# Kernel optimization log

Measured on AMD Instinct MI355X. Metric: run time of the kernel, lower is better.

The kernel has to match this reference:

```python
import jax, jax.numpy as jnp
import numpy as np

D_MODEL, N_HEADS, LATENT, ROPE = 4096, 128, 512, 64
HEAD_DIM = D_MODEL // N_HEADS  # 32
B, S = 2, 1024


def setup_inputs() -> dict:
    key = jax.random.key(0)
    ks = jax.random.split(key, 9)
    def w(k, i, o):
        return jax.random.normal(k, (i, o), dtype=jnp.float32) * (1.0 / np.sqrt(i))
    return {
        "x": jax.random.normal(ks[0], (B, S, D_MODEL), dtype=jnp.float32),
        "Wq_down": w(ks[1], D_MODEL, LATENT),
        "Wq_up": w(ks[2], LATENT, N_HEADS * HEAD_DIM),
        "Wq_rope": w(ks[3], D_MODEL, N_HEADS * ROPE),
        "Wkv_down": w(ks[4], D_MODEL, LATENT),
        "Wk_up": w(ks[5], LATENT, N_HEADS * HEAD_DIM),
        "Wv_up": w(ks[6], LATENT, N_HEADS * HEAD_DIM),
        "Wk_rope": w(ks[7], D_MODEL, ROPE),
        "Wo": w(ks[8], N_HEADS * HEAD_DIM, D_MODEL),
    }


def reference(x, Wq_down, Wq_up, Wq_rope, Wkv_down, Wk_up, Wv_up, Wk_rope, Wo):
    b, s, _ = x.shape
    # latent down-projections
    c_q = x @ Wq_down                                   # [B,S,latent]
    c_kv = x @ Wkv_down                                 # [B,S,latent]
    # up-projections, reshaped to per-head
    q_c = (c_q @ Wq_up).reshape(b, s, N_HEADS, HEAD_DIM)    # [B,S,H,Dh]
    q_r = (x @ Wq_rope).reshape(b, s, N_HEADS, ROPE)        # [B,S,H,Dr]
    k_c = (c_kv @ Wk_up).reshape(b, s, N_HEADS, HEAD_DIM)   # [B,S,H,Dh]
    v_c = (c_kv @ Wv_up).reshape(b, s, N_HEADS, HEAD_DIM)   # [B,S,H,Dh]
    k_r = x @ Wk_rope                                       # [B,S,Dr] shared over heads
    scale = jnp.asarray((HEAD_DIM + ROPE) ** 0.5, x.dtype)
    # scores = q.k with q=[q_c|q_r], k=[k_c|k_r(broadcast)] -> split the dot product
    scores = (jnp.einsum("bqhd,bkhd->bhqk", q_c, k_c)
              + jnp.einsum("bqhd,bkd->bhqk", q_r, k_r)) / scale  # [B,H,S,S]
    attn = jax.nn.softmax(scores, axis=-1)
    out = jnp.einsum("bhqk,bkhd->bqhd", attn, v_c)          # [B,S,H,Dh]
    out = out.reshape(b, s, N_HEADS * HEAD_DIM)
    return out @ Wo                                         # [B,S,d_model]
```

## Files before the change

kernel.cpp:

```cpp
#include <hip/hip_runtime.h>
#include <hip/hip_bf16.h>
#include <math.h>

#define D_MODEL 4096
#define N_HEADS 128
#define LATENT  512
#define ROPE_D  64
#define HEAD_D  32
#define BATCH   2
#define SEQ     1024
#define NTOK    (BATCH*SEQ)

typedef unsigned short u16;
typedef __attribute__((ext_vector_type(8))) short bf16x8;
typedef __attribute__((ext_vector_type(4))) float f32x4;

__device__ __forceinline__ u16 f2bf(float f) {
    union { float f; unsigned u; } v; v.f = f;
    unsigned r = (v.u + 0x7fffu + ((v.u >> 16) & 1u)) >> 16;
    return (u16)r;
}

__device__ __forceinline__ void gl_lds16(const u16* g, u16* l) {
    __builtin_amdgcn_global_load_lds(
        (const __attribute__((address_space(1))) unsigned int*)g,
        (__attribute__((address_space(3))) unsigned int*)l, 16, 0, 0);
}

__device__ __forceinline__ void castT_tile(const float* __restrict__ W,
                                           u16* __restrict__ Wt,
                                           int K, int N, int jx, int jy,
                                           float (*tile)[33])
{
    const int tid = threadIdx.x;
    const int j0 = jx * 32, i0 = jy * 32;
    {
        int r = tid >> 3, c4 = (tid & 7) << 2;
        float4 v = *(const float4*)(W + (size_t)(i0 + r) * N + j0 + c4);
        tile[r][c4 + 0] = v.x; tile[r][c4 + 1] = v.y;
        tile[r][c4 + 2] = v.z; tile[r][c4 + 3] = v.w;
    }
    __syncthreads();
    {
        int n = tid >> 3, k4 = (tid & 7) << 2;
        u16 o[4] = { f2bf(tile[k4 + 0][n]), f2bf(tile[k4 + 1][n]),
                     f2bf(tile[k4 + 2][n]), f2bf(tile[k4 + 3][n]) };
        *(uint2*)(Wt + (size_t)(j0 + n) * K + i0 + k4) = *(uint2*)o;
    }
}

__device__ __forceinline__ void gemm_core(const u16* __restrict__ A,
                                          const u16* __restrict__ Bt,
                                          void* __restrict__ Cout,
                                          int N, int K, int lda, int ldb, int ldc,
                                          int bm, int bn, u16* As, u16* Bs,
                                          int OUTF32)
{
    const int tid  = threadIdx.x;
    const int lane = tid & 63;
    const int wave = tid >> 6;
    const int wr = wave >> 1, wc = wave & 1;
    const int l15 = lane & 15, lg = lane >> 4;

    f32x4 acc[4][4];
    #pragma unroll
    for (int i = 0; i < 4; ++i)
        #pragma unroll
        for (int j = 0; j < 4; ++j) acc[i][j] = (f32x4){0.f, 0.f, 0.f, 0.f};

    for (int kt = 0; kt < K; kt += 64) {
        __syncthreads();
        #pragma unroll
        for (int i = 0; i < 4; ++i) {
            int f = i * 256 + tid;
            int row = f >> 3, c = f & 7;
            int sc = c ^ (row & 7);
            gl_lds16(A + (size_t)(bm + row) * lda + kt + sc * 8, As + f * 8);
        }
        #pragma unroll
        for (int i = 0; i < 4; ++i) {
            int f = i * 256 + tid;
            int row = f >> 3, c = f & 7;
            int sc = c ^ (row & 7);
            gl_lds16(Bt + (size_t)(bn + row) * ldb + kt + sc * 8, Bs + f * 8);
        }
        __syncthreads();

        #pragma unroll
        for (int t = 0; t < 2; ++t) {
            bf16x8 af[4], bf[4];
            #pragma unroll
            for (int fm = 0; fm < 4; ++fm) {
                int row = wr * 64 + fm * 16 + l15;
                int c = (t * 4 + lg) ^ (row & 7);
                af[fm] = *(const bf16x8*)(As + row * 64 + c * 8);
            }
            #pragma unroll
            for (int fn = 0; fn < 4; ++fn) {
                int row = wc * 64 + fn * 16 + l15;
                int c = (t * 4 + lg) ^ (row & 7);
                bf[fn] = *(const bf16x8*)(Bs + row * 64 + c * 8);
            }
            #pragma unroll
            for (int fm = 0; fm < 4; ++fm)
                #pragma unroll
                for (int fn = 0; fn < 4; ++fn)
                    acc[fm][fn] = __builtin_amdgcn_mfma_f32_16x16x32_bf16(
                        af[fm], bf[fn], acc[fm][fn], 0, 0, 0);
        }
    }

    #pragma unroll
    for (int fm = 0; fm < 4; ++fm)
        #pragma unroll
        for (int fn = 0; fn < 4; ++fn)
            #pragma unroll
            for (int ri = 0; ri < 4; ++ri) {
                int row = bm + wr * 64 + fm * 16 + 4 * lg + ri;
                int col = bn + wc * 64 + fn * 16 + l15;
                float v = acc[fm][fn][ri];
                if (OUTF32) ((float*)Cout)[(size_t)row * ldc + col] = v;
                else        ((u16*)Cout)[(size_t)row * ldc + col] = f2bf(v);
            }
}

template<int OUTF32>
__global__ __launch_bounds__(256)
void gemm_bf16(const u16* __restrict__ A, const u16* __restrict__ Bt,
               void* __restrict__ Cout, int N, int K,
               int lda, int ldb, int ldc)
{
    __shared__ __align__(16) u16 As[128 * 64];
    __shared__ __align__(16) u16 Bs[128 * 64];
    const int nwg  = gridDim.x * gridDim.y;
    const int orig = blockIdx.y * gridDim.x + blockIdx.x;
    const int swz  = (orig & 7) * (nwg >> 3) + (orig >> 3);
    const int bm = (swz % gridDim.y) * 128;
    const int bn = (swz / gridDim.y) * 128;
    gemm_core(A, Bt, Cout, N, K, lda, ldb, ldc, bm, bn, As, Bs, OUTF32);
}

__global__ __launch_bounds__(256)
void prep_kernel(const float* __restrict__ x, u16* __restrict__ xb,
                 const float* __restrict__ Wq_rope, const float* __restrict__ Wq_down,
                 const float* __restrict__ Wkv_down, const float* __restrict__ Wk_rope,
                 const float* __restrict__ Wk_up, const float* __restrict__ Wv_up,
                 const float* __restrict__ Wq_up,
                 u16* __restrict__ BigT, u16* __restrict__ UpT, u16* __restrict__ WuqT)
{
    __shared__ float tile[32][33];
    const int tid = threadIdx.x;
    int id = blockIdx.x;
    if (id < 4096) {
        size_t i = ((size_t)id * 256 + tid) * 8;
        float4 a = *(const float4*)(x + i);
        float4 b = *(const float4*)(x + i + 4);
        u16 o[8] = {f2bf(a.x), f2bf(a.y), f2bf(a.z), f2bf(a.w),
                    f2bf(b.x), f2bf(b.y), f2bf(b.z), f2bf(b.w)};
        *(bf16x8*)(xb + i) = *(bf16x8*)o;
        return;
    }
    id -= 4096;
    if (id < 32768) { castT_tile(Wq_rope, BigT, 4096, 8192, id & 255, id >> 8, tile); return; }
    id -= 32768;
    if (id < 2048) { castT_tile(Wq_down, BigT + (size_t)8192 * 4096, 4096, 512, id & 15, id >> 4, tile); return; }
    id -= 2048;
    if (id < 2048) { castT_tile(Wkv_down, BigT + (size_t)8704 * 4096, 4096, 512, id & 15, id >> 4, tile); return; }
    id -= 2048;
    if (id < 256) { castT_tile(Wk_rope, BigT + (size_t)9216 * 4096, 4096, 64, id & 1, id >> 1, tile); return; }
    id -= 256;
    if (id < 2048) { castT_tile(Wk_up, UpT, 512, 4096, id & 127, id >> 7, tile); return; }
    id -= 2048;
    if (id < 2048) { castT_tile(Wv_up, UpT + (size_t)4096 * 512, 512, 4096, id & 127, id >> 7, tile); return; }
    id -= 2048;
    if (id < 2048) { castT_tile(Wq_up, WuqT, 512, 4096, id & 127, id >> 7, tile); return; }
    id -= 2048;
    {
        u16* dst = BigT + ((size_t)9280 + id) * 4096;
        bf16x8 z = (bf16x8){0, 0, 0, 0, 0, 0, 0, 0};
        *(bf16x8*)(dst + tid * 8) = z;
        *(bf16x8*)(dst + 2048 + tid * 8) = z;
    }
}

__global__ __launch_bounds__(256)
void fused2_kernel(const u16* __restrict__ Cbig, const u16* __restrict__ UpT,
                   u16* __restrict__ C2, const u16* __restrict__ WuqT,
                   u16* __restrict__ q_c, const float* __restrict__ Wo,
                   u16* __restrict__ WoT)
{
    __shared__ __align__(16) u16 As[128 * 64];
    __shared__ __align__(16) u16 Bs[128 * 64];
    int id = blockIdx.x;
    if (id < 1024) {
        const int swz = (id & 7) * 128 + (id >> 3);
        const int bm = (swz & 15) * 128, bn = (swz >> 4) * 128;
        gemm_core(Cbig + 8704, UpT, C2, 8192, 512, 9344, 512, 8192, bm, bn, As, Bs, 0);
        return;
    }
    id -= 1024;
    if (id < 512) {
        const int swz = (id & 7) * 64 + (id >> 3);
        const int bm = (swz & 15) * 128, bn = (swz >> 4) * 128;
        gemm_core(Cbig + 8192, WuqT, q_c, 4096, 512, 9344, 512, 4096, bm, bn, As, Bs, 0);
        return;
    }
    id -= 512;
    {
        float (*tile)[33] = reinterpret_cast<float(*)[33]>(As);
        castT_tile(Wo, WoT, 4096, 4096, id & 127, id >> 7, tile);
    }
}

__global__ __launch_bounds__(256)
void vtrans_kernel(const u16* __restrict__ vc, u16* __restrict__ vt)
{
    __shared__ __align__(16) u16 tile[64][72];
    const int tid = threadIdx.x;
    const int c0 = blockIdx.x * 64;
    const int s0 = blockIdx.y * 64;
    const int b  = blockIdx.z;
    #pragma unroll
    for (int it = 0; it < 2; ++it) {
        int e = it * 256 + tid;
        int r = e >> 3, c8 = e & 7;
        *(bf16x8*)&tile[r][c8 * 8] =
            *(const bf16x8*)(vc + (size_t)(b * SEQ + s0 + r) * 8192 + c0 + c8 * 8);
    }
    __syncthreads();
    #pragma unroll
    for (int it = 0; it < 2; ++it) {
        int e = it * 256 + tid;
        int d = e >> 3, c8 = e & 7;
        u16 o[8];
        #pragma unroll
        for (int j = 0; j < 8; ++j) o[j] = tile[c8 * 8 + j][d];
        *(bf16x8*)(vt + (size_t)(b * D_MODEL + c0 + d) * SEQ + s0 + c8 * 8) = *(bf16x8*)o;
    }
}

__global__ __launch_bounds__(256)
void attn_kernel(const u16* __restrict__ q_c, const u16* __restrict__ q_r,
                 const u16* __restrict__ k_c, const u16* __restrict__ k_r,
                 const u16* __restrict__ vt,  u16* __restrict__ attn_out)
{
    __shared__ __align__(16) u16 s_kc[2][64 * 32];
    __shared__ __align__(16) u16 s_kr[2][64 * 64];
    __shared__ __align__(16) u16 s_vt[2][32 * 64];
    __shared__ __align__(16) u16 s_p[4][16 * 64];

    const int tid  = threadIdx.x;
    const int lane = tid & 63;
    const int w    = tid >> 6;
    const int l15  = lane & 15, lg = lane >> 4;
    const int q0 = blockIdx.x * 64;
    const int h  = blockIdx.y;
    const int b  = blockIdx.z;
    const size_t bS = (size_t)b * SEQ;
    const int hc = h * HEAD_D;
    const float c2 = 0.1020620726159658f * 1.44269504088896f;

    const int qrow = q0 + w * 16 + l15;
    const bf16x8 qf0 = *(const bf16x8*)(q_c + (bS + qrow) * 4096 + hc + lg * 8);
    const bf16x8 qf1 = *(const bf16x8*)(q_r + (bS + qrow) * 9344 + h * ROPE_D + lg * 8);
    const bf16x8 qf2 = *(const bf16x8*)(q_r + (bS + qrow) * 9344 + h * ROPE_D + 32 + lg * 8);

    float m2 = -1e30f, lsum = 0.f;
    f32x4 oacc[2];
    oacc[0] = (f32x4){0.f, 0.f, 0.f, 0.f};
    oacc[1] = (f32x4){0.f, 0.f, 0.f, 0.f};

    auto stage = [&](int buf, int k0) {
        { int f = tid, r = f >> 2, c = f & 3;
          gl_lds16(k_c + (bS + k0 + r) * 8192 + hc + ((c ^ (r & 3)) << 3),
                   &s_kc[buf][f * 8]); }
        #pragma unroll
        for (int it = 0; it < 2; ++it) {
          int f = it * 256 + tid, r = f >> 3, c = f & 7;
          gl_lds16(k_r + (bS + k0 + r) * 9344 + ((c ^ (r & 7)) << 3),
                   &s_kr[buf][f * 8]); }
        { int f = tid, d = f >> 3, c = f & 7;
          gl_lds16(vt + ((size_t)b * D_MODEL + hc + d) * SEQ + k0 + ((c ^ (d & 7)) << 3),
                   &s_vt[buf][f * 8]); }
    };

    stage(0, 0);
    asm volatile("s_waitcnt vmcnt(0)" ::: "memory");
    __builtin_amdgcn_sched_barrier(0);
    __builtin_amdgcn_s_barrier();
    __builtin_amdgcn_sched_barrier(0);

    int cur = 0;
    for (int t = 0; t < SEQ / 64; ++t) {
        if (t + 1 < SEQ / 64) {
            stage(cur ^ 1, (t + 1) * 64);
            asm volatile("s_waitcnt vmcnt(4)" ::: "memory");
        } else {
            asm volatile("s_waitcnt vmcnt(0)" ::: "memory");
        }
        __builtin_amdgcn_sched_barrier(0);
        __builtin_amdgcn_s_barrier();
        __builtin_amdgcn_sched_barrier(0);

        f32x4 sc[4];
        #pragma unroll
        for (int fc = 0; fc < 4; ++fc) sc[fc] = (f32x4){0.f, 0.f, 0.f, 0.f};
        __builtin_amdgcn_s_setprio(1);
        #pragma unroll
        for (int fc = 0; fc < 4; ++fc) {
            int row = fc * 16 + l15;
            bf16x8 kb = *(const bf16x8*)&s_kc[cur][row * 32 + ((lg ^ (row & 3)) << 3)];
            sc[fc] = __builtin_amdgcn_mfma_f32_16x16x32_bf16(kb, qf0, sc[fc], 0, 0, 0);
        }
        #pragma unroll
        for (int tt = 0; tt < 2; ++tt) {
            bf16x8 qf = tt ? qf2 : qf1;
            #pragma unroll
            for (int fc = 0; fc < 4; ++fc) {
                int row = fc * 16 + l15;
                bf16x8 kb = *(const bf16x8*)&s_kr[cur][row * 64 + (((tt * 4 + lg) ^ (row & 7)) << 3)];
                sc[fc] = __builtin_amdgcn_mfma_f32_16x16x32_bf16(kb, qf, sc[fc], 0, 0, 0);
            }
        }
        __builtin_amdgcn_s_setprio(0);

        float tmx = sc[0][0];
        #pragma unroll
        for (int fc = 0; fc < 4; ++fc)
            #pragma unroll
            for (int ri = 0; ri < 4; ++ri)
                tmx = fmaxf(tmx, sc[fc][ri]);
        tmx = fmaxf(tmx, __shfl_xor(tmx, 16));
        tmx = fmaxf(tmx, __shfl_xor(tmx, 32));
        float tl2 = tmx * c2;
        if (!__all(tl2 <= m2 + 8.f)) {
            float mn = fmaxf(m2, tl2);
            float corr = exp2f(m2 - mn);
            m2 = mn;
            lsum *= corr;
            #pragma unroll
            for (int ri = 0; ri < 4; ++ri) {
                float cr = __shfl(corr, 4 * lg + ri);
                oacc[0][ri] *= cr; oacc[1][ri] *= cr;
            }
        }
        float rs = 0.f;
        unsigned pk0[4], pk1[4];
        #pragma unroll
        for (int fc = 0; fc < 4; ++fc) {
            float p0 = exp2f(fmaf(sc[fc][0], c2, -m2));
            float p1 = exp2f(fmaf(sc[fc][1], c2, -m2));
            float p2 = exp2f(fmaf(sc[fc][2], c2, -m2));
            float p3 = exp2f(fmaf(sc[fc][3], c2, -m2));
            rs += (p0 + p1) + (p2 + p3);
            asm("v_cvt_pk_bf16_f32 %0, %1, %2" : "=v"(pk0[fc]) : "v"(p0), "v"(p1));
            asm("v_cvt_pk_bf16_f32 %0, %1, %2" : "=v"(pk1[fc]) : "v"(p2), "v"(p3));
        }
        rs += __shfl_xor(rs, 16);
        rs += __shfl_xor(rs, 32);
        lsum += rs;
        #pragma unroll
        for (int fc = 0; fc < 4; ++fc) {
            int ch = (2 * fc + (lg >> 1)) ^ (l15 & 7);
            *(uint2*)&s_p[w][l15 * 64 + ch * 8 + 4 * (lg & 1)] =
                make_uint2(pk0[fc], pk1[fc]);
        }

        __builtin_amdgcn_s_setprio(1);
        #pragma unroll
        for (int t2 = 0; t2 < 2; ++t2) {
            bf16x8 pa = *(const bf16x8*)&s_p[w][l15 * 64 + (((t2 * 4 + lg) ^ (l15 & 7)) << 3)];
            #pragma unroll
            for (int fd = 0; fd < 2; ++fd) {
                int row = fd * 16 + l15;
                bf16x8 vb = *(const bf16x8*)&s_vt[cur][row * 64 + (((t2 * 4 + lg) ^ (row & 7)) << 3)];
                oacc[fd] = __builtin_amdgcn_mfma_f32_16x16x32_bf16(pa, vb, oacc[fd], 0, 0, 0);
            }
        }
        __builtin_amdgcn_s_setprio(0);

        asm volatile("s_waitcnt lgkmcnt(0)" ::: "memory");
        __builtin_amdgcn_sched_barrier(0);
        __builtin_amdgcn_s_barrier();
        __builtin_amdgcn_sched_barrier(0);
        cur ^= 1;
    }

    #pragma unroll
    for (int ri = 0; ri < 4; ++ri) {
        float ls = __shfl(lsum, 4 * lg + ri);
        float inv = 1.f / ls;
        int row = q0 + w * 16 + 4 * lg + ri;
        attn_out[(bS + row) * 4096 + hc + l15]      = f2bf(oacc[0][ri] * inv);
        attn_out[(bS + row) * 4096 + hc + 16 + l15] = f2bf(oacc[1][ri] * inv);
    }
}

extern "C" void kernel_launch(void* const* d_in, const int* in_sizes, int n_in,
                              void* d_out, int out_size, void* d_ws, size_t ws_size,
                              hipStream_t stream)
{
    (void)in_sizes; (void)n_in; (void)out_size; (void)ws_size;

    const float* x        = (const float*)d_in[0];
    const float* Wq_down  = (const float*)d_in[1];
    const float* Wq_up    = (const float*)d_in[2];
    const float* Wq_rope  = (const float*)d_in[3];
    const float* Wkv_down = (const float*)d_in[4];
    const float* Wk_up    = (const float*)d_in[5];
    const float* Wv_up    = (const float*)d_in[6];
    const float* Wk_rope  = (const float*)d_in[7];
    const float* Wo       = (const float*)d_in[8];

    u16* ws   = (u16*)d_ws;
    u16* xb   = ws;
    u16* BigT = xb + (size_t)8388608;
    u16* UpT  = BigT + (size_t)38797312;
    u16* WuqT = UpT + (size_t)4194304;
    u16* C_big= WuqT + (size_t)2097152;
    u16* C2   = C_big + (size_t)19136512;
    u16* WoT  = BigT;
    u16* vt   = BigT + (size_t)16777216;
    u16* q_c  = BigT + (size_t)25165824;
    u16* attn_out = xb;

    dim3 blk(256);

    hipLaunchKernelGGL(prep_kernel, dim3(47424), blk, 0, stream,
                       x, xb, Wq_rope, Wq_down, Wkv_down, Wk_rope,
                       Wk_up, Wv_up, Wq_up, BigT, UpT, WuqT);
    gemm_bf16<0><<<dim3(73, 16), blk, 0, stream>>>(
        xb, BigT, C_big, 9344, 4096, 4096, 4096, 9344);
    hipLaunchKernelGGL(fused2_kernel, dim3(1024 + 512 + 16384), blk, 0, stream,
                       C_big, UpT, C2, WuqT, q_c, Wo, WoT);
    hipLaunchKernelGGL(vtrans_kernel, dim3(64, 16, 2), blk, 0, stream, C2 + 4096, vt);
    hipLaunchKernelGGL(attn_kernel, dim3(16, 128, 2), blk, 0, stream,
                       q_c, C_big, C2, C_big + 9216, vt, attn_out);
    gemm_bf16<1><<<dim3(32, 16), blk, 0, stream>>>(
        attn_out, WoT, d_out, 4096, 4096, 4096, 4096, 4096);
}
```

Baseline: 512.7 us.

## Fuse V transpose into up-projection GEMM epilogue and drop vtrans kernel

The K/V up-projection GEMM now writes K directly into a compact 4096-wide buffer and writes V already transposed into the vt layout from its epilogue. This removes the separate vtrans kernel launch along with its extra read and write of V. The attention kernel's K row stride changes to match. The transposed V stores are 8-byte scattered writes along the sequence dimension, which may coalesce less well. The tile max reduction in attention is also rewritten as a shallower tree.

```diff
diff --git a/kernel.cpp b/kernel.cpp
--- a/kernel.cpp
+++ b/kernel.cpp
@@ -49,12 +49,13 @@
     }
 }
 
+template<int MODE>
 __device__ __forceinline__ void gemm_core(const u16* __restrict__ A,
                                           const u16* __restrict__ Bt,
                                           void* __restrict__ Cout,
                                           int N, int K, int lda, int ldb, int ldc,
                                           int bm, int bn, u16* As, u16* Bs,
-                                          int OUTF32)
+                                          u16* __restrict__ vtp)
 {
     const int tid  = threadIdx.x;
     const int lane = tid & 63;
@@ -113,18 +114,38 @@
     #pragma unroll
     for (int fm = 0; fm < 4; ++fm)
         #pragma unroll
-        for (int fn = 0; fn < 4; ++fn)
-            #pragma unroll
-            for (int ri = 0; ri < 4; ++ri) {
-                int row = bm + wr * 64 + fm * 16 + 4 * lg + ri;
-                int col = bn + wc * 64 + fn * 16 + l15;
-                float v = acc[fm][fn][ri];
-                if (OUTF32) ((float*)Cout)[(size_t)row * ldc + col] = v;
-                else        ((u16*)Cout)[(size_t)row * ldc + col] = f2bf(v);
-            }
-}
-
-template<int OUTF32>
+        for (int fn = 0; fn < 4; ++fn) {
+            int row0 = bm + wr * 64 + fm * 16 + 4 * lg;
+            int col  = bn + wc * 64 + fn * 16 + l15;
+            if (MODE == 2) {
+                if (col < 4096) {
+                    #pragma unroll
+                    for (int ri = 0; ri < 4; ++ri)
+                        ((u16*)Cout)[(size_t)(row0 + ri) * 4096 + col] =
+                            f2bf(acc[fm][fn][ri]);
+                } else {
+                    int d = col - 4096;
+                    int b = row0 >> 10, s = row0 & 1023;
+                    u16 o[4] = {f2bf(acc[fm][fn][0]), f2bf(acc[fm][fn][1]),
+                                f2bf(acc[fm][fn][2]), f2bf(acc[fm][fn][3])};
+                    *(uint2*)(vtp + ((size_t)b * 4096 + d) * 1024 + s) = *(uint2*)o;
+                }
+            } else {
+                if (col < N) {
+                    #pragma unroll
+                    for (int ri = 0; ri < 4; ++ri) {
+                        float v = acc[fm][fn][ri];
+                        if (MODE == 1)
+                            ((float*)Cout)[(size_t)(row0 + ri) * ldc + col] = v;
+                        else
+                            ((u16*)Cout)[(size_t)(row0 + ri) * ldc + col] = f2bf(v);
+                    }
+                }
+            }
+        }
+}
+
+template<int MODE>
 __global__ __launch_bounds__(256)
 void gemm_bf16(const u16* __restrict__ A, const u16* __restrict__ Bt,
                void* __restrict__ Cout, int N, int K,
@@ -137,7 +158,7 @@
     const int swz  = (orig & 7) * (nwg >> 3) + (orig >> 3);
     const int bm = (swz % gridDim.y) * 128;
     const int bn = (swz / gridDim.y) * 128;
-    gemm_core(A, Bt, Cout, N, K, lda, ldb, ldc, bm, bn, As, Bs, OUTF32);
+    gemm_core<MODE>(A, Bt, Cout, N, K, lda, ldb, ldc, bm, bn, As, Bs, nullptr);
 }
 
 __global__ __launch_bounds__(256)
@@ -185,9 +206,9 @@
 
 __global__ __launch_bounds__(256)
 void fused2_kernel(const u16* __restrict__ Cbig, const u16* __restrict__ UpT,
-                   u16* __restrict__ C2, const u16* __restrict__ WuqT,
-                   u16* __restrict__ q_c, const float* __restrict__ Wo,
-                   u16* __restrict__ WoT)
+                   u16* __restrict__ k_c, u16* __restrict__ vt,
+                   const u16* __restrict__ WuqT, u16* __restrict__ q_c,
+                   const float* __restrict__ Wo, u16* __restrict__ WoT)
 {
     __shared__ __align__(16) u16 As[128 * 64];
     __shared__ __align__(16) u16 Bs[128 * 64];
@@ -195,47 +216,20 @@
     if (id < 1024) {
         const int swz = (id & 7) * 128 + (id >> 3);
         const int bm = (swz & 15) * 128, bn = (swz >> 4) * 128;
-        gemm_core(Cbig + 8704, UpT, C2, 8192, 512, 9344, 512, 8192, bm, bn, As, Bs, 0);
+        gemm_core<2>(Cbig + 8704, UpT, k_c, 8192, 512, 9344, 512, 4096, bm, bn, As, Bs, vt);
         return;
     }
     id -= 1024;
     if (id < 512) {
         const int swz = (id & 7) * 64 + (id >> 3);
         const int bm = (swz & 15) * 128, bn = (swz >> 4) * 128;
-        gemm_core(Cbig + 8192, WuqT, q_c, 4096, 512, 9344, 512, 4096, bm, bn, As, Bs, 0);
+        gemm_core<0>(Cbig + 8192, WuqT, q_c, 4096, 512, 9344, 512, 4096, bm, bn, As, Bs, nullptr);
         return;
     }
     id -= 512;
     {
         float (*tile)[33] = reinterpret_cast<float(*)[33]>(As);
         castT_tile(Wo, WoT, 4096, 4096, id & 127, id >> 7, tile);
-    }
-}
-
-__global__ __launch_bounds__(256)
-void vtrans_kernel(const u16* __restrict__ vc, u16* __restrict__ vt)
-{
-    __shared__ __align__(16) u16 tile[64][72];
-    const int tid = threadIdx.x;
-    const int c0 = blockIdx.x * 64;
-    const int s0 = blockIdx.y * 64;
-    const int b  = blockIdx.z;
-    #pragma unroll
-    for (int it = 0; it < 2; ++it) {
-        int e = it * 256 + tid;
-        int r = e >> 3, c8 = e & 7;
-        *(bf16x8*)&tile[r][c8 * 8] =
-            *(const bf16x8*)(vc + (size_t)(b * SEQ + s0 + r) * 8192 + c0 + c8 * 8);
-    }
-    __syncthreads();
-    #pragma unroll
-    for (int it = 0; it < 2; ++it) {
-        int e = it * 256 + tid;
-        int d = e >> 3, c8 = e & 7;
-        u16 o[8];
-        #pragma unroll
-        for (int j = 0; j < 8; ++j) o[j] = tile[c8 * 8 + j][d];
-        *(bf16x8*)(vt + (size_t)(b * D_MODEL + c0 + d) * SEQ + s0 + c8 * 8) = *(bf16x8*)o;
     }
 }
 
@@ -272,7 +266,7 @@
 
     auto stage = [&](int buf, int k0) {
         { int f = tid, r = f >> 2, c = f & 3;
-          gl_lds16(k_c + (bS + k0 + r) * 8192 + hc + ((c ^ (r & 3)) << 3),
+          gl_lds16(k_c + (bS + k0 + r) * 4096 + hc + ((c ^ (r & 3)) << 3),
                    &s_kc[buf][f * 8]); }
         #pragma unroll
         for (int it = 0; it < 2; ++it) {
@@ -324,12 +318,14 @@
         }
         __builtin_amdgcn_s_setprio(0);
 
-        float tmx = sc[0][0];
-        #pragma unroll
-        for (int fc = 0; fc < 4; ++fc)
-            #pragma unroll
-            for (int ri = 0; ri < 4; ++ri)
-                tmx = fmaxf(tmx, sc[fc][ri]);
+        float a0 = fmaxf(fmaxf(sc[0][0], sc[0][1]), sc[0][2]);
+        float a1 = fmaxf(fmaxf(sc[0][3], sc[1][0]), sc[1][1]);
+        float a2 = fmaxf(fmaxf(sc[1][2], sc[1][3]), sc[2][0]);
+        float a3 = fmaxf(fmaxf(sc[2][1], sc[2][2]), sc[2][3]);
+        float a4 = fmaxf(fmaxf(sc[3][0], sc[3][1]), sc[3][2]);
+        float b0 = fmaxf(fmaxf(a0, a1), a2);
+        float b1 = fmaxf(fmaxf(a3, a4), sc[3][3]);
+        float tmx = fmaxf(b0, b1);
         tmx = fmaxf(tmx, __shfl_xor(tmx, 16));
         tmx = fmaxf(tmx, __shfl_xor(tmx, 32));
         float tl2 = tmx * c2;
@@ -418,7 +414,7 @@
     u16* UpT  = BigT + (size_t)38797312;
     u16* WuqT = UpT + (size_t)4194304;
     u16* C_big= WuqT + (size_t)2097152;
-    u16* C2   = C_big + (size_t)19136512;
+    u16* kc   = C_big + (size_t)19136512;
     u16* WoT  = BigT;
     u16* vt   = BigT + (size_t)16777216;
     u16* q_c  = BigT + (size_t)25165824;
@@ -432,10 +428,9 @@
     gemm_bf16<0><<<dim3(73, 16), blk, 0, stream>>>(
         xb, BigT, C_big, 9344, 4096, 4096, 4096, 9344);
     hipLaunchKernelGGL(fused2_kernel, dim3(1024 + 512 + 16384), blk, 0, stream,
-                       C_big, UpT, C2, WuqT, q_c, Wo, WoT);
-    hipLaunchKernelGGL(vtrans_kernel, dim3(64, 16, 2), blk, 0, stream, C2 + 4096, vt);
+                       C_big, UpT, kc, vt, WuqT, q_c, Wo, WoT);
     hipLaunchKernelGGL(attn_kernel, dim3(16, 128, 2), blk, 0, stream,
-                       q_c, C_big, C2, C_big + 9216, vt, attn_out);
+                       q_c, C_big, kc, C_big + 9216, vt, attn_out);
     gemm_bf16<1><<<dim3(32, 16), blk, 0, stream>>>(
         attn_out, WoT, d_out, 4096, 4096, 4096, 4096, 4096);
 }
```

Result: slower. 527.2 us (+2.8%).

## Add 256x256 multi-buffered GEMM for the big fused projection and split off remainder

Applied to the files above, without the earlier changes.

Adds a new 512-thread GEMM kernel with 256x256 tiles and a four-slot LDS ring of K-halves, loaded asynchronously via global_load_lds with explicit vmcnt waits and barriers. It covers the first 8192 columns of the large x-projection, and the remaining 1152 columns go to the existing 128x128 kernel, which gains a column bound check. Larger tiles raise data reuse per LDS load and overlap loads with MFMA work, at the cost of 128KB of LDS per block, low occupancy, and only 256 blocks. The attention row-max reduction is also rewritten as a tree to shorten the dependency chain.

```diff
diff --git a/kernel.cpp b/kernel.cpp
--- a/kernel.cpp
+++ b/kernel.cpp
@@ -49,12 +49,12 @@
     }
 }
 
+template<int MODE>
 __device__ __forceinline__ void gemm_core(const u16* __restrict__ A,
                                           const u16* __restrict__ Bt,
                                           void* __restrict__ Cout,
                                           int N, int K, int lda, int ldb, int ldc,
-                                          int bm, int bn, u16* As, u16* Bs,
-                                          int OUTF32)
+                                          int bm, int bn, u16* As, u16* Bs)
 {
     const int tid  = threadIdx.x;
     const int lane = tid & 63;
@@ -118,13 +118,15 @@
             for (int ri = 0; ri < 4; ++ri) {
                 int row = bm + wr * 64 + fm * 16 + 4 * lg + ri;
                 int col = bn + wc * 64 + fn * 16 + l15;
-                float v = acc[fm][fn][ri];
-                if (OUTF32) ((float*)Cout)[(size_t)row * ldc + col] = v;
-                else        ((u16*)Cout)[(size_t)row * ldc + col] = f2bf(v);
-            }
-}
-
-template<int OUTF32>
+                if (col < N) {
+                    float v = acc[fm][fn][ri];
+                    if (MODE == 1) ((float*)Cout)[(size_t)row * ldc + col] = v;
+                    else           ((u16*)Cout)[(size_t)row * ldc + col] = f2bf(v);
+                }
+            }
+}
+
+template<int MODE>
 __global__ __launch_bounds__(256)
 void gemm_bf16(const u16* __restrict__ A, const u16* __restrict__ Bt,
                void* __restrict__ Cout, int N, int K,
@@ -137,7 +139,123 @@
     const int swz  = (orig & 7) * (nwg >> 3) + (orig >> 3);
     const int bm = (swz % gridDim.y) * 128;
     const int bn = (swz / gridDim.y) * 128;
-    gemm_core(A, Bt, Cout, N, K, lda, ldb, ldc, bm, bn, As, Bs, OUTF32);
+    gemm_core<MODE>(A, Bt, Cout, N, K, lda, ldb, ldc, bm, bn, As, Bs);
+}
+
+__global__ __launch_bounds__(512)
+void gemm256(const u16* __restrict__ A, const u16* __restrict__ Bt,
+             u16* __restrict__ Cout, int N, int K,
+             int lda, int ldb, int ldc)
+{
+    constexpr int SLOT = 16384;
+    extern __shared__ __align__(16) u16 lds[];
+
+    const int tid  = threadIdx.x;
+    const int lane = tid & 63, wave = tid >> 6;
+    const int wr = wave >> 2, wc = wave & 3;
+    const int l15 = lane & 15, lg = lane >> 4;
+
+    const int nwg  = gridDim.x * gridDim.y;
+    const int orig = blockIdx.y * gridDim.x + blockIdx.x;
+    const int swz  = (orig & 7) * (nwg >> 3) + (orig >> 3);
+    const int bm = (swz % gridDim.y) * 256;
+    const int bn = (swz / gridDim.y) * 256;
+
+    const int NH = K >> 5;
+    const int NT = NH >> 1;
+
+    auto stage_unit = [&](int u) {
+        const int h = u >> 1, op = u & 1;
+        u16* base = lds + (h & 3) * SLOT + op * 8192;
+        const u16* G = op ? Bt : A;
+        const int ldg  = op ? ldb : lda;
+        const int boff = op ? bn : bm;
+        const int kh = h << 5;
+        #pragma unroll
+        for (int it = 0; it < 2; ++it) {
+            int f = it * 512 + tid;
+            int row = f >> 2, c = f & 3;
+            int gc = c ^ ((row >> 1) & 3);
+            gl_lds16(G + (size_t)(boff + row) * ldg + kh + gc * 8, base + f * 8);
+        }
+    };
+
+    f32x4 acc[8][4];
+    #pragma unroll
+    for (int m = 0; m < 8; ++m)
+        #pragma unroll
+        for (int n = 0; n < 4; ++n) acc[m][n] = (f32x4){0.f, 0.f, 0.f, 0.f};
+
+    #pragma unroll
+    for (int u = 0; u < 6; ++u) stage_unit(u);
+    asm volatile("s_waitcnt vmcnt(4)" ::: "memory");
+    __builtin_amdgcn_sched_barrier(0);
+    __builtin_amdgcn_s_barrier();
+    __builtin_amdgcn_sched_barrier(0);
+
+    for (int t = 0; t < NT; ++t) {
+        #pragma unroll
+        for (int hh = 0; hh < 2; ++hh) {
+            const int h = 2 * t + hh;
+            const u16* As_ = lds + (h & 3) * SLOT;
+            const u16* Bs_ = As_ + 8192;
+            bf16x8 bfr[4];
+            #pragma unroll
+            for (int sub = 0; sub < 2; ++sub) {
+                bf16x8 af[4];
+                #pragma unroll
+                for (int mm = 0; mm < 4; ++mm) {
+                    int row = wr * 128 + (sub * 4 + mm) * 16 + l15;
+                    af[mm] = *(const bf16x8*)(As_ + row * 32 +
+                                              ((lg ^ ((row >> 1) & 3)) << 3));
+                }
+                if (sub == 0) {
+                    #pragma unroll
+                    for (int nn = 0; nn < 4; ++nn) {
+                        int row = wc * 64 + nn * 16 + l15;
+                        bfr[nn] = *(const bf16x8*)(Bs_ + row * 32 +
+                                                   ((lg ^ ((row >> 1) & 3)) << 3));
+                    }
+                }
+                {
+                    int u = 4 * t + 6 + 2 * hh + sub;
+                    if (u < 2 * NH) stage_unit(u);
+                }
+                if (hh == 1 && sub == 1 && t + 1 < NT) {
+                    int iss = 4 * t + 10; if (iss > 2 * NH) iss = 2 * NH;
+                    int ru = iss - (4 * t + 8);
+                    if (ru >= 2) asm volatile("s_waitcnt vmcnt(4)" ::: "memory");
+                    else         asm volatile("s_waitcnt vmcnt(0)" ::: "memory");
+                }
+                __builtin_amdgcn_sched_barrier(0);
+                __builtin_amdgcn_s_barrier();
+                __builtin_amdgcn_sched_barrier(0);
+                __builtin_amdgcn_s_setprio(1);
+                #pragma unroll
+                for (int mm = 0; mm < 4; ++mm)
+                    #pragma unroll
+                    for (int nn = 0; nn < 4; ++nn)
+                        acc[sub * 4 + mm][nn] = __builtin_amdgcn_mfma_f32_16x16x32_bf16(
+                            af[mm], bfr[nn], acc[sub * 4 + mm][nn], 0, 0, 0);
+                __builtin_amdgcn_s_setprio(0);
+                __builtin_amdgcn_sched_barrier(0);
+                __builtin_amdgcn_s_barrier();
+                __builtin_amdgcn_sched_barrier(0);
+            }
+        }
+    }
+
+    #pragma unroll
+    for (int m = 0; m < 8; ++m)
+        #pragma unroll
+        for (int n = 0; n < 4; ++n)
+            #pragma unroll
+            for (int ri = 0; ri < 4; ++ri) {
+                int row = bm + wr * 128 + m * 16 + 4 * lg + ri;
+                int col = bn + wc * 64 + n * 16 + l15;
+                if (col < N)
+                    Cout[(size_t)row * ldc + col] = f2bf(acc[m][n][ri]);
+            }
 }
 
 __global__ __launch_bounds__(256)
@@ -195,14 +313,14 @@
     if (id < 1024) {
         const int swz = (id & 7) * 128 + (id >> 3);
         const int bm = (swz & 15) * 128, bn = (swz >> 4) * 128;
-        gemm_core(Cbig + 8704, UpT, C2, 8192, 512, 9344, 512, 8192, bm, bn, As, Bs, 0);
+        gemm_core<0>(Cbig + 8704, UpT, C2, 8192, 512, 9344, 512, 8192, bm, bn, As, Bs);
         return;
     }
     id -= 1024;
     if (id < 512) {
         const int swz = (id & 7) * 64 + (id >> 3);
         const int bm = (swz & 15) * 128, bn = (swz >> 4) * 128;
-        gemm_core(Cbig + 8192, WuqT, q_c, 4096, 512, 9344, 512, 4096, bm, bn, As, Bs, 0);
+        gemm_core<0>(Cbig + 8192, WuqT, q_c, 4096, 512, 9344, 512, 4096, bm, bn, As, Bs);
         return;
     }
     id -= 512;
@@ -324,12 +442,14 @@
         }
         __builtin_amdgcn_s_setprio(0);
 
-        float tmx = sc[0][0];
-        #pragma unroll
-        for (int fc = 0; fc < 4; ++fc)
-            #pragma unroll
-            for (int ri = 0; ri < 4; ++ri)
-                tmx = fmaxf(tmx, sc[fc][ri]);
+        float a0 = fmaxf(fmaxf(sc[0][0], sc[0][1]), sc[0][2]);
+        float a1 = fmaxf(fmaxf(sc[0][3], sc[1][0]), sc[1][1]);
+        float a2 = fmaxf(fmaxf(sc[1][2], sc[1][3]), sc[2][0]);
+        float a3 = fmaxf(fmaxf(sc[2][1], sc[2][2]), sc[2][3]);
+        float a4 = fmaxf(fmaxf(sc[3][0], sc[3][1]), sc[3][2]);
+        float b0 = fmaxf(fmaxf(a0, a1), a2);
+        float b1 = fmaxf(fmaxf(a3, a4), sc[3][3]);
+        float tmx = fmaxf(b0, b1);
         tmx = fmaxf(tmx, __shfl_xor(tmx, 16));
         tmx = fmaxf(tmx, __shfl_xor(tmx, 32));
         float tl2 = tmx * c2;
@@ -426,11 +546,16 @@
 
     dim3 blk(256);
 
+    (void)hipFuncSetAttribute((const void*)&gemm256,
+                              hipFuncAttributeMaxDynamicSharedMemorySize, 131072);
+
     hipLaunchKernelGGL(prep_kernel, dim3(47424), blk, 0, stream,
                        x, xb, Wq_rope, Wq_down, Wkv_down, Wk_rope,
                        Wk_up, Wv_up, Wq_up, BigT, UpT, WuqT);
-    gemm_bf16<0><<<dim3(73, 16), blk, 0, stream>>>(
-        xb, BigT, C_big, 9344, 4096, 4096, 4096, 9344);
+    gemm256<<<dim3(32, 8), dim3(512), 131072, stream>>>(
+        xb, BigT, C_big, 8192, 4096, 4096, 4096, 9344);
+    gemm_bf16<0><<<dim3(9, 16), blk, 0, stream>>>(
+        xb, BigT + (size_t)8192 * 4096, C_big + 8192, 1152, 4096, 4096, 4096, 9344);
     hipLaunchKernelGGL(fused2_kernel, dim3(1024 + 512 + 16384), blk, 0, stream,
                        C_big, UpT, C2, WuqT, q_c, Wo, WoT);
     hipLaunchKernelGGL(vtrans_kernel, dim3(64, 16, 2), blk, 0, stream, C2 + 4096, vt);
```

New measurement: 540.4 us. 1.05x slower.

## Compute softmax row sums via MFMA against ones column; change K-LDS swizzle

Applied to the files above, without the earlier changes.

Drops the per-tile VALU row-sum and its cross-lane shuffles in the attention kernel. The softmax denominator is now accumulated by an extra MFMA of the probability tile against an LDS ones matrix, so it sums the bf16-rounded probabilities used in P·V. The s_kc swizzle now uses (row>>1)&3 to cut LDS bank conflicts, and the tile max becomes a shallower tree. The GEMM core also gains a column bound check and a template mode parameter. The cost is one more MFMA and one more LDS read per inner step, plus a small extra LDS buffer.

```diff
diff --git a/kernel.cpp b/kernel.cpp
--- a/kernel.cpp
+++ b/kernel.cpp
@@ -49,12 +49,12 @@
     }
 }
 
+template<int MODE>
 __device__ __forceinline__ void gemm_core(const u16* __restrict__ A,
                                           const u16* __restrict__ Bt,
                                           void* __restrict__ Cout,
                                           int N, int K, int lda, int ldb, int ldc,
-                                          int bm, int bn, u16* As, u16* Bs,
-                                          int OUTF32)
+                                          int bm, int bn, u16* As, u16* Bs)
 {
     const int tid  = threadIdx.x;
     const int lane = tid & 63;
@@ -118,13 +118,15 @@
             for (int ri = 0; ri < 4; ++ri) {
                 int row = bm + wr * 64 + fm * 16 + 4 * lg + ri;
                 int col = bn + wc * 64 + fn * 16 + l15;
-                float v = acc[fm][fn][ri];
-                if (OUTF32) ((float*)Cout)[(size_t)row * ldc + col] = v;
-                else        ((u16*)Cout)[(size_t)row * ldc + col] = f2bf(v);
-            }
-}
-
-template<int OUTF32>
+                if (col < N) {
+                    float v = acc[fm][fn][ri];
+                    if (MODE == 1) ((float*)Cout)[(size_t)row * ldc + col] = v;
+                    else           ((u16*)Cout)[(size_t)row * ldc + col] = f2bf(v);
+                }
+            }
+}
+
+template<int MODE>
 __global__ __launch_bounds__(256)
 void gemm_bf16(const u16* __restrict__ A, const u16* __restrict__ Bt,
                void* __restrict__ Cout, int N, int K,
@@ -137,7 +139,7 @@
     const int swz  = (orig & 7) * (nwg >> 3) + (orig >> 3);
     const int bm = (swz % gridDim.y) * 128;
     const int bn = (swz / gridDim.y) * 128;
-    gemm_core(A, Bt, Cout, N, K, lda, ldb, ldc, bm, bn, As, Bs, OUTF32);
+    gemm_core<MODE>(A, Bt, Cout, N, K, lda, ldb, ldc, bm, bn, As, Bs);
 }
 
 __global__ __launch_bounds__(256)
@@ -195,14 +197,14 @@
     if (id < 1024) {
         const int swz = (id & 7) * 128 + (id >> 3);
         const int bm = (swz & 15) * 128, bn = (swz >> 4) * 128;
-        gemm_core(Cbig + 8704, UpT, C2, 8192, 512, 9344, 512, 8192, bm, bn, As, Bs, 0);
+        gemm_core<0>(Cbig + 8704, UpT, C2, 8192, 512, 9344, 512, 8192, bm, bn, As, Bs);
         return;
     }
     id -= 1024;
     if (id < 512) {
         const int swz = (id & 7) * 64 + (id >> 3);
         const int bm = (swz & 15) * 128, bn = (swz >> 4) * 128;
-        gemm_core(Cbig + 8192, WuqT, q_c, 4096, 512, 9344, 512, 4096, bm, bn, As, Bs, 0);
+        gemm_core<0>(Cbig + 8192, WuqT, q_c, 4096, 512, 9344, 512, 4096, bm, bn, As, Bs);
         return;
     }
     id -= 512;
@@ -248,6 +250,7 @@
     __shared__ __align__(16) u16 s_kr[2][64 * 64];
     __shared__ __align__(16) u16 s_vt[2][32 * 64];
     __shared__ __align__(16) u16 s_p[4][16 * 64];
+    __shared__ __align__(16) u16 s_one[16 * 64];
 
     const int tid  = threadIdx.x;
     const int lane = tid & 63;
@@ -265,14 +268,15 @@
     const bf16x8 qf1 = *(const bf16x8*)(q_r + (bS + qrow) * 9344 + h * ROPE_D + lg * 8);
     const bf16x8 qf2 = *(const bf16x8*)(q_r + (bS + qrow) * 9344 + h * ROPE_D + 32 + lg * 8);
 
-    float m2 = -1e30f, lsum = 0.f;
-    f32x4 oacc[2];
+    float m2 = -1e30f;
+    f32x4 oacc[3];
     oacc[0] = (f32x4){0.f, 0.f, 0.f, 0.f};
     oacc[1] = (f32x4){0.f, 0.f, 0.f, 0.f};
+    oacc[2] = (f32x4){0.f, 0.f, 0.f, 0.f};
 
     auto stage = [&](int buf, int k0) {
         { int f = tid, r = f >> 2, c = f & 3;
-          gl_lds16(k_c + (bS + k0 + r) * 8192 + hc + ((c ^ (r & 3)) << 3),
+          gl_lds16(k_c + (bS + k0 + r) * 8192 + hc + ((c ^ ((r >> 1) & 3)) << 3),
                    &s_kc[buf][f * 8]); }
         #pragma unroll
         for (int it = 0; it < 2; ++it) {
@@ -284,8 +288,12 @@
                    &s_vt[buf][f * 8]); }
     };
 
+    {
+        unsigned v = (tid < 16) ? 0x3F803F80u : 0u;
+        *(uint2*)&s_one[tid * 4] = make_uint2(v, v);
+    }
     stage(0, 0);
-    asm volatile("s_waitcnt vmcnt(0)" ::: "memory");
+    asm volatile("s_waitcnt vmcnt(0) lgkmcnt(0)" ::: "memory");
     __builtin_amdgcn_sched_barrier(0);
     __builtin_amdgcn_s_barrier();
     __builtin_amdgcn_sched_barrier(0);
@@ -309,7 +317,7 @@
         #pragma unroll
         for (int fc = 0; fc < 4; ++fc) {
             int row = fc * 16 + l15;
-            bf16x8 kb = *(const bf16x8*)&s_kc[cur][row * 32 + ((lg ^ (row & 3)) << 3)];
+            bf16x8 kb = *(const bf16x8*)&s_kc[cur][row * 32 + ((lg ^ ((row >> 1) & 3)) << 3)];
             sc[fc] = __builtin_amdgcn_mfma_f32_16x16x32_bf16(kb, qf0, sc[fc], 0, 0, 0);
         }
         #pragma unroll
@@ -324,12 +332,14 @@
         }
         __builtin_amdgcn_s_setprio(0);
 
-        float tmx = sc[0][0];
-        #pragma unroll
-        for (int fc = 0; fc < 4; ++fc)
-            #pragma unroll
-            for (int ri = 0; ri < 4; ++ri)
-                tmx = fmaxf(tmx, sc[fc][ri]);
+        float a0 = fmaxf(fmaxf(sc[0][0], sc[0][1]), sc[0][2]);
+        float a1 = fmaxf(fmaxf(sc[0][3], sc[1][0]), sc[1][1]);
+        float a2 = fmaxf(fmaxf(sc[1][2], sc[1][3]), sc[2][0]);
+        float a3 = fmaxf(fmaxf(sc[2][1], sc[2][2]), sc[2][3]);
+        float a4 = fmaxf(fmaxf(sc[3][0], sc[3][1]), sc[3][2]);
+        float b0 = fmaxf(fmaxf(a0, a1), a2);
+        float b1 = fmaxf(fmaxf(a3, a4), sc[3][3]);
+        float tmx = fmaxf(b0, b1);
         tmx = fmaxf(tmx, __shfl_xor(tmx, 16));
         tmx = fmaxf(tmx, __shfl_xor(tmx, 32));
         float tl2 = tmx * c2;
@@ -337,14 +347,12 @@
             float mn = fmaxf(m2, tl2);
             float corr = exp2f(m2 - mn);
             m2 = mn;
-            lsum *= corr;
             #pragma unroll
             for (int ri = 0; ri < 4; ++ri) {
                 float cr = __shfl(corr, 4 * lg + ri);
-                oacc[0][ri] *= cr; oacc[1][ri] *= cr;
-            }
-        }
-        float rs = 0.f;
+                oacc[0][ri] *= cr; oacc[1][ri] *= cr; oacc[2][ri] *= cr;
+            }
+        }
         unsigned pk0[4], pk1[4];
         #pragma unroll
         for (int fc = 0; fc < 4; ++fc) {
@@ -352,13 +360,9 @@
             float p1 = exp2f(fmaf(sc[fc][1], c2, -m2));
             float p2 = exp2f(fmaf(sc[fc][2], c2, -m2));
             float p3 = exp2f(fmaf(sc[fc][3], c2, -m2));
-            rs += (p0 + p1) + (p2 + p3);
             asm("v_cvt_pk_bf16_f32 %0, %1, %2" : "=v"(pk0[fc]) : "v"(p0), "v"(p1));
             asm("v_cvt_pk_bf16_f32 %0, %1, %2" : "=v"(pk1[fc]) : "v"(p2), "v"(p3));
         }
-        rs += __shfl_xor(rs, 16);
-        rs += __shfl_xor(rs, 32);
-        lsum += rs;
         #pragma unroll
         for (int fc = 0; fc < 4; ++fc) {
             int ch = (2 * fc + (lg >> 1)) ^ (l15 & 7);
@@ -376,6 +380,8 @@
                 bf16x8 vb = *(const bf16x8*)&s_vt[cur][row * 64 + (((t2 * 4 + lg) ^ (row & 7)) << 3)];
                 oacc[fd] = __builtin_amdgcn_mfma_f32_16x16x32_bf16(pa, vb, oacc[fd], 0, 0, 0);
             }
+            bf16x8 vb1 = *(const bf16x8*)&s_one[l15 * 64 + (((t2 * 4 + lg) ^ (l15 & 7)) << 3)];
+            oacc[2] = __builtin_amdgcn_mfma_f32_16x16x32_bf16(pa, vb1, oacc[2], 0, 0, 0);
         }
         __builtin_amdgcn_s_setprio(0);
 
@@ -388,7 +394,7 @@
 
     #pragma unroll
     for (int ri = 0; ri < 4; ++ri) {
-        float ls = __shfl(lsum, 4 * lg + ri);
+        float ls = __shfl(oacc[2][ri], lg << 4);
         float inv = 1.f / ls;
         int row = q0 + w * 16 + 4 * lg + ri;
         attn_out[(bS + row) * 4096 + hc + l15]      = f2bf(oacc[0][ri] * inv);
```

Result: no change. 522.3 us (+1.9%).
